# Kernel optimization log

Measured on AMD Instinct MI355X. Metric: run time of the kernel, lower is better.

## Reference

```python
import jax, jax.numpy as jnp
import numpy as np

N = 200000      # total points
B = 4           # number of point clouds
C_IN = 128
C_OUT = 256
GRID = 0.05
EPS = 1e-5      # BatchNorm eps


def setup_inputs() -> dict:
    key = jax.random.key(0)
    ks = jax.random.split(key, 9)
    xyz = jax.random.uniform(ks[0], (1, N, 3), dtype=jnp.float32)
    features = jax.random.normal(ks[1], (1, N, C_IN), dtype=jnp.float32)
    offset = jnp.array([50000, 100000, 150000, 200000], dtype=jnp.int32)
    W1 = jax.random.normal(ks[2], (C_OUT, C_IN), dtype=jnp.float32) * 0.02
    b1 = jax.random.normal(ks[3], (C_OUT,), dtype=jnp.float32) * 0.01
    gamma = jax.random.uniform(ks[4], (C_OUT,), dtype=jnp.float32, minval=0.5, maxval=1.5)
    beta = jax.random.normal(ks[5], (C_OUT,), dtype=jnp.float32) * 0.1
    W2 = jax.random.normal(ks[6], (C_OUT, C_OUT), dtype=jnp.float32) * 0.02
    b2 = jax.random.normal(ks[7], (C_OUT,), dtype=jnp.float32) * 0.01
    return {"xyz": xyz, "features": features, "offset": offset,
            "W1": W1, "b1": b1, "gamma": gamma, "beta": beta, "W2": W2, "b2": b2}


def _offset2batch(offset, n):
    counts = jnp.diff(jnp.concatenate([jnp.zeros((1,), offset.dtype), offset]))
    return jnp.repeat(jnp.arange(offset.shape[0], dtype=jnp.int32), counts,
                      total_repeat_length=n)


def reference(xyz, features, offset, W1, b1, gamma, beta, W2, b2):
    pos = xyz[0]          # [N, 3]
    x = features[0]       # [N, C_IN]
    batch = _offset2batch(offset, pos.shape[0])  # [N]

    # fc: 1x1 conv == linear; BatchNorm1d in training mode (batch stats, biased var)
    h = x @ W1.T + b1                                   # [N, C_OUT]
    mu = h.mean(axis=0)
    var = h.var(axis=0)
    h = (h - mu) / jnp.sqrt(var + EPS) * gamma + beta
    h = jax.nn.relu(h)
    feats = h @ W2.T + b2                               # [N, C_OUT]

    # per-batch min corner (start)
    start = jax.ops.segment_min(pos, batch, num_segments=B)   # [B, 3]

    # voxel grid clustering
    coords = jnp.floor((pos - start[batch]) / GRID).astype(jnp.int32)  # [N, 3] >= 0
    dims = coords.max(axis=0) + 1
    lin = ((batch * dims[0] + coords[:, 0]) * dims[1] + coords[:, 1]) * dims[2] + coords[:, 2]

    uniq, inv, counts = jnp.unique(lin, return_inverse=True, return_counts=True)
    M = uniq.shape[0]

    # segment_csr mean / max over voxels (order-independent, equals sorted CSR reduce)
    xyz_out = jax.ops.segment_sum(pos, inv, num_segments=M) / counts[:, None].astype(pos.dtype)
    feat_out = jax.ops.segment_max(feats, inv, num_segments=M)

    seg_batch = jax.ops.segment_max(batch, inv, num_segments=M)
    offset_out = jnp.cumsum(jnp.bincount(seg_batch, length=B)).astype(offset.dtype)

    return (xyz_out[None], feat_out[None], offset_out, inv)
```

## Files before the change

kernel.cpp:

```cpp
#include <hip/hip_runtime.h>
#include <stdint.h>

#define GRID_SZ 0.05f
#define BN_EPS 1e-5f

typedef __attribute__((ext_vector_type(8))) short bf16x8;
typedef __attribute__((ext_vector_type(4))) float f32x4;

#define WS_START   0
#define WS_DIMS    64
#define WS_CHSUM   128
#define WS_CHSQ    1152
#define WS_AC      2176
#define WS_BC      3200
#define WS_W1B     4224
#define WS_W2B     69760
#define WS_GRAM    200832
#define WS_CSUM    266368
#define WS_HIST    266880
#define WS_RANK    529024
#define WS_CURS    791296
#define WS_BSUM    1053440
#define WS_XYZS    1053952
#define WS_LIN     1840384
#define WS_PERM    2640384
#define WS_XB      3440384

__device__ __forceinline__ short f2bf(float f) {
  unsigned u = __float_as_uint(f);
  u += 0x7FFFu + ((u >> 16) & 1u);
  return (short)(u >> 16);
}

__device__ __forceinline__ bf16x8 load_frag(const float* p) {
  f32x4 a = *(const f32x4*)p;
  f32x4 b = *(const f32x4*)(p + 4);
  bf16x8 r;
  r[0] = f2bf(a[0]); r[1] = f2bf(a[1]); r[2] = f2bf(a[2]); r[3] = f2bf(a[3]);
  r[4] = f2bf(b[0]); r[5] = f2bf(b[1]); r[6] = f2bf(b[2]); r[7] = f2bf(b[3]);
  return r;
}

__device__ __forceinline__ int batch_of(int p, const int* offs, int nb) {
  int b = 0;
  while (b < nb - 1 && p >= offs[b]) b++;
  return b;
}

__global__ void k_conv(const float* __restrict__ src, short* __restrict__ dst, size_t n8) {
  size_t i = (size_t)blockIdx.x * blockDim.x + threadIdx.x;
  size_t stride = (size_t)gridDim.x * blockDim.x;
  for (; i < n8; i += stride)
    *(bf16x8*)(dst + i * 8) = load_frag(src + i * 8);
}

__global__ void k_convw(const float* __restrict__ W1, const float* __restrict__ W2,
                        short* __restrict__ W1b, short* __restrict__ W2b) {
  int i = blockIdx.x * blockDim.x + threadIdx.x;
  if (i < 4096) *(bf16x8*)(W1b + i * 8) = load_frag(W1 + i * 8);
  else { int j = i - 4096; *(bf16x8*)(W2b + j * 8) = load_frag(W2 + j * 8); }
}

__global__ void k_init(unsigned* featU, size_t featN, int* hist, float* xyzs,
                       float* chsum, float* chsq, float* gram, float* csum,
                       unsigned* gstart, int* gdims) {
  size_t i = (size_t)blockIdx.x * blockDim.x + threadIdx.x;
  size_t stride = (size_t)gridDim.x * blockDim.x;
  for (size_t j = i; j < featN; j += stride) featU[j] = 0u;
  for (size_t j = i; j < 65536; j += stride) hist[j] = 0;
  for (size_t j = i; j < 65536u * 3; j += stride) xyzs[j] = 0.f;
  for (size_t j = i; j < 16384; j += stride) gram[j] = 0.f;
  if (i < 256) { chsum[i] = 0.f; chsq[i] = 0.f; }
  if (i < 128) csum[i] = 0.f;
  if (i < 12) gstart[i] = 0x7F800000u;
  if (i < 3) gdims[i] = 0;
}

__global__ void k_min(const float* __restrict__ pos, const int* __restrict__ offs,
                      int N, int nb, unsigned* gstart) {
  __shared__ unsigned smin[12];
  int tid = threadIdx.x;
  if (tid < 12) smin[tid] = 0x7F800000u;
  __syncthreads();
  int p = blockIdx.x * blockDim.x + tid;
  if (p < N) {
    int b = batch_of(p, offs, nb);
    for (int c = 0; c < 3; c++)
      atomicMin(&smin[b * 3 + c], __float_as_uint(pos[p * 3 + c]));
  }
  __syncthreads();
  if (tid < 3 * nb) atomicMin(&gstart[tid], smin[tid]);
}

__global__ void k_dims(const float* __restrict__ pos, const int* __restrict__ offs,
                       int N, int nb, const unsigned* gstart, int* gdims) {
  __shared__ int sd[3];
  int tid = threadIdx.x;
  if (tid < 3) sd[tid] = 0;
  __syncthreads();
  int p = blockIdx.x * blockDim.x + tid;
  if (p < N) {
    int b = batch_of(p, offs, nb);
    for (int c = 0; c < 3; c++) {
      float s = __uint_as_float(gstart[b * 3 + c]);
      int cc = (int)floorf((pos[p * 3 + c] - s) / GRID_SZ);
      atomicMax(&sd[c], cc);
    }
  }
  __syncthreads();
  if (tid < 3) atomicMax(&gdims[tid], sd[tid]);
}

__global__ void k_hist(const float* __restrict__ pos, const int* __restrict__ offs,
                       int N, int nb, const unsigned* gstart, const int* gdims,
                       int* lin, int* hist, float* xyzs) {
  int p = blockIdx.x * blockDim.x + threadIdx.x;
  if (p >= N) return;
  int b = batch_of(p, offs, nb);
  int d0 = gdims[0] + 1, d1 = gdims[1] + 1, d2 = gdims[2] + 1;
  int c[3];
  for (int i = 0; i < 3; i++) {
    float s = __uint_as_float(gstart[b * 3 + i]);
    c[i] = (int)floorf((pos[p * 3 + i] - s) / GRID_SZ);
  }
  int li = ((b * d0 + c[0]) * d1 + c[1]) * d2 + c[2];
  if (li < 0 || li >= 65536) li = 0;
  lin[p] = li;
  atomicAdd(&hist[li], 1);
  atomicAdd(&xyzs[li * 3 + 0], pos[p * 3 + 0]);
  atomicAdd(&xyzs[li * 3 + 1], pos[p * 3 + 1]);
  atomicAdd(&xyzs[li * 3 + 2], pos[p * 3 + 2]);
}

__global__ __launch_bounds__(1024) void k_scanA(const int* __restrict__ hist,
                                                const int* __restrict__ gdims, int nb,
                                                int2* bsum) {
  __shared__ int so[16], sc2[16];
  int d0 = gdims[0] + 1, d1 = gdims[1] + 1, d2 = gdims[2] + 1;
  int bins = nb * d0 * d1 * d2;
  if (bins > 65536) bins = 65536;
  int i = blockIdx.x * 1024 + threadIdx.x;
  int o = 0, c = 0;
  if (i < bins) { int h = hist[i]; o = (h > 0); c = h; }
  for (int d = 1; d < 64; d <<= 1) { o += __shfl_xor(o, d); c += __shfl_xor(c, d); }
  int w = threadIdx.x >> 6;
  if ((threadIdx.x & 63) == 0) { so[w] = o; sc2[w] = c; }
  __syncthreads();
  if (threadIdx.x == 0) {
    int O = 0, C = 0;
    for (int k = 0; k < 16; k++) { O += so[k]; C += sc2[k]; }
    bsum[blockIdx.x] = make_int2(O, C);
  }
}

__global__ __launch_bounds__(1024) void k_scanB(const int* __restrict__ hist,
                                                const int* __restrict__ gdims, int nb,
                                                const int2* __restrict__ bsum,
                                                int* rank, int* cursor) {
  __shared__ int so[1024], sc2[1024];
  __shared__ int sbase[2];
  int d0 = gdims[0] + 1, d1 = gdims[1] + 1, d2 = gdims[2] + 1;
  int bins = nb * d0 * d1 * d2;
  if (bins > 65536) bins = 65536;
  int b = blockIdx.x;
  int tid = threadIdx.x;
  if (tid == 0) {
    int O = 0, C = 0;
    for (int k = 0; k < b; k++) { int2 s = bsum[k]; O += s.x; C += s.y; }
    sbase[0] = O; sbase[1] = C;
  }
  int i = b * 1024 + tid;
  int h = (i < bins) ? hist[i] : 0;
  int o = (h > 0), c = h;
  so[tid] = o; sc2[tid] = c;
  __syncthreads();
  for (int off = 1; off < 1024; off <<= 1) {
    int vo = (tid >= off) ? so[tid - off] : 0;
    int vc = (tid >= off) ? sc2[tid - off] : 0;
    __syncthreads();
    so[tid] += vo; sc2[tid] += vc;
    __syncthreads();
  }
  if (i < bins) {
    rank[i]   = sbase[0] + so[tid] - o;
    cursor[i] = sbase[1] + sc2[tid] - c;
  }
  if (i == bins - 1) rank[bins] = sbase[0] + so[tid];
}

__global__ void k_scatter(const int* __restrict__ lin, const int* __restrict__ rank,
                          int* cursor, int N, int* __restrict__ perm,
                          float* __restrict__ out_inv) {
  int p = blockIdx.x * blockDim.x + threadIdx.x;
  if (p >= N) return;
  int li = lin[p];
  out_inv[p] = (float)rank[li];
  int slot = atomicAdd(&cursor[li], 1);
  perm[slot] = p;
}

__global__ void k_voxfin(const int* __restrict__ hist, const int* __restrict__ rank,
                         const float* __restrict__ xyzs, const int* __restrict__ gdims,
                         int nb, float* out_xyz, float* out_off) {
  int d0 = gdims[0] + 1, d1 = gdims[1] + 1, d2 = gdims[2] + 1;
  int dxyz = d0 * d1 * d2;
  int bins = nb * dxyz;
  if (bins > 65536) bins = 65536;
  int i = blockIdx.x * blockDim.x + threadIdx.x;
  if (blockIdx.x == 0 && (int)threadIdx.x < nb) {
    int t = (int)threadIdx.x;
    int idx = (t + 1) * dxyz; if (idx > bins) idx = bins;
    out_off[t] = (float)rank[idx];
  }
  if (i >= bins) return;
  int cnt = hist[i];
  if (cnt <= 0) return;
  int v = rank[i];
  float fc = (float)cnt;
  out_xyz[v * 3 + 0] = xyzs[i * 3 + 0] / fc;
  out_xyz[v * 3 + 1] = xyzs[i * 3 + 1] / fc;
  out_xyz[v * 3 + 2] = xyzs[i * 3 + 2] / fc;
}

#define GCHUNK 1024
__global__ __launch_bounds__(256, 2) void k_gram(const short* __restrict__ Xb, int N,
                                                 float* __restrict__ gram,
                                                 float* __restrict__ csum) {
  __shared__ short xt[128 * 72];
  __shared__ float lcs[128];
  int tid = threadIdx.x;
  int wid = tid >> 6, lane = tid & 63;
  int lr = lane & 15, lg = lane >> 4;
  int base = blockIdx.x * GCHUNK;
  int cg = tid & 7;
  float cs[16];
#pragma unroll
  for (int j = 0; j < 16; j++) cs[j] = 0.f;
  f32x4 acc[2][8];
#pragma unroll
  for (int a = 0; a < 2; a++)
#pragma unroll
    for (int b = 0; b < 8; b++) acc[a][b] = (f32x4){0.f, 0.f, 0.f, 0.f};

  for (int k0 = 0; k0 < GCHUNK; k0 += 64) {
    __syncthreads();
#pragma unroll
    for (int it = 0; it < 2; it++) {
      int task = tid + it * 256;
      int r = task >> 3;
      int row = base + k0 + r;
      bf16x8 v0 = {0,0,0,0,0,0,0,0}, v1 = {0,0,0,0,0,0,0,0};
      if (row < N) {
        const short* src = Xb + (size_t)row * 128 + cg * 16;
        v0 = *(const bf16x8*)src;
        v1 = *(const bf16x8*)(src + 8);
      }
#pragma unroll
      for (int j = 0; j < 8; j++) {
        cs[j]     += __uint_as_float(((unsigned)(unsigned short)v0[j]) << 16);
        cs[j + 8] += __uint_as_float(((unsigned)(unsigned short)v1[j]) << 16);
      }
      int rs = r ^ (cg << 3);
#pragma unroll
      for (int j = 0; j < 8; j++) {
        xt[(cg * 16 + j) * 72 + rs]     = v0[j];
        xt[(cg * 16 + 8 + j) * 72 + rs] = v1[j];
      }
    }
    __syncthreads();
#pragma unroll
    for (int ks = 0; ks < 2; ks++) {
      int kk = ks * 32 + lg * 8;
      bf16x8 f[8], af[2];
#pragma unroll
      for (int s = 0; s < 8; s++)
        f[s] = *(const bf16x8*)(xt + (s * 16 + lr) * 72 + (kk ^ (s << 3)));
#pragma unroll
      for (int a = 0; a < 2; a++) {
        int ti = wid * 2 + a;
        af[a] = *(const bf16x8*)(xt + (ti * 16 + lr) * 72 + (kk ^ (ti << 3)));
      }
#pragma unroll
      for (int a = 0; a < 2; a++)
#pragma unroll
        for (int b = 0; b < 8; b++)
          acc[a][b] = __builtin_amdgcn_mfma_f32_16x16x32_bf16(af[a], f[b], acc[a][b], 0, 0, 0);
    }
  }
#pragma unroll
  for (int a = 0; a < 2; a++)
#pragma unroll
    for (int b = 0; b < 8; b++)
#pragma unroll
      for (int r_ = 0; r_ < 4; r_++) {
        int ci = (wid * 2 + a) * 16 + lg * 4 + r_;
        int cj = b * 16 + lr;
        atomicAdd(&gram[ci * 128 + cj], acc[a][b][r_]);
      }
  if (tid < 128) lcs[tid] = 0.f;
  __syncthreads();
#pragma unroll
  for (int j = 0; j < 16; j++) atomicAdd(&lcs[cg * 16 + j], cs[j]);
  __syncthreads();
  if (tid < 128) atomicAdd(&csum[tid], lcs[tid]);
}

__global__ __launch_bounds__(128) void k_finalizeG(const float* __restrict__ gram,
                                                   const float* __restrict__ csum,
                                                   const float* __restrict__ W1,
                                                   const float* __restrict__ b1,
                                                   const float* __restrict__ gamma,
                                                   const float* __restrict__ beta,
                                                   int N, float* Ac, float* Bc) {
  __shared__ float w[128], red[128], red2[128];
  int c = blockIdx.x, j = threadIdx.x;
  w[j] = W1[c * 128 + j];
  __syncthreads();
  float t = 0.f;
  for (int k = 0; k < 128; k++) t += gram[k * 128 + j] * w[k];
  red[j]  = t * w[j];
  red2[j] = w[j] * csum[j];
  __syncthreads();
  for (int off = 64; off > 0; off >>= 1) {
    if (j < off) { red[j] += red[j + off]; red2[j] += red2[j + off]; }
    __syncthreads();
  }
  if (j == 0) {
    float fn = (float)N;
    float q  = red[0] / fn;
    float md = red2[0] / fn;
    float b  = b1[c];
    float mu = md + b;
    float e2 = q + 2.f * b * md + b * b;
    float var = e2 - mu * mu;
    float s = gamma[c] * rsqrtf(var + BN_EPS);
    Ac[c] = s;
    Bc[c] = (b - mu) * s + beta[c];
  }
}

template <bool XBF>
__global__ __launch_bounds__(256) void k_statsA(const float* __restrict__ X,
                                                const short* __restrict__ Xb,
                                                const short* __restrict__ W1b,
                                                const float* __restrict__ b1, int N,
                                                float* chsum, float* chsq) {
  int tid = threadIdx.x;
  int wid = tid >> 6, lane = tid & 63;
  int lr = lane & 15, lg = lane >> 4;
  int p0 = blockIdx.x * 64;
  int wcol = wid * 64;
  f32x4 acc[4][4] = {};
  for (int kk = 0; kk < 4; kk++) {
    int k = kk * 32 + lg * 8;
    bf16x8 af[4], bfr[4];
    for (int m = 0; m < 4; m++) {
      int row = p0 + m * 16 + lr; if (row >= N) row = N - 1;
      if (XBF) af[m] = *(const bf16x8*)(Xb + (size_t)row * 128 + k);
      else     af[m] = load_frag(X + (size_t)row * 128 + k);
    }
    for (int n = 0; n < 4; n++)
      bfr[n] = *(const bf16x8*)(W1b + (size_t)(wcol + n * 16 + lr) * 128 + k);
    for (int m = 0; m < 4; m++)
      for (int n = 0; n < 4; n++)
        acc[m][n] = __builtin_amdgcn_mfma_f32_16x16x32_bf16(af[m], bfr[n], acc[m][n], 0, 0, 0);
  }
  for (int n = 0; n < 4; n++) {
    int c = wcol + n * 16 + lr;
    float bv = b1[c];
    float s1 = 0.f, s2 = 0.f;
    for (int m = 0; m < 4; m++)
      for (int r = 0; r < 4; r++) {
        int row = p0 + m * 16 + lg * 4 + r;
        if (row < N) {
          float h = acc[m][n][r] + bv;
          s1 += h; s2 += h * h;
        }
      }
    s1 += __shfl_xor(s1, 16); s2 += __shfl_xor(s2, 16);
    s1 += __shfl_xor(s1, 32); s2 += __shfl_xor(s2, 32);
    if (lg == 0) { atomicAdd(&chsum[c], s1); atomicAdd(&chsq[c], s2); }
  }
}

__global__ void k_finalize(const float* chsum, const float* chsq, const float* b1,
                           const float* gamma, const float* beta, int N,
                           float* Ac, float* Bc) {
  int c = threadIdx.x;
  float fn = (float)N;
  float mu = chsum[c] / fn;
  float var = chsq[c] / fn - mu * mu;
  float s = gamma[c] * rsqrtf(var + BN_EPS);
  Ac[c] = s;
  Bc[c] = (b1[c] - mu) * s + beta[c];
}

template <bool XBF>
__global__ __launch_bounds__(256, 4) void k_gemmB(const float* __restrict__ X,
                                                  const short* __restrict__ Xb,
                                                  const short* __restrict__ W1b,
                                                  const short* __restrict__ W2b,
                                                  const float* __restrict__ b2,
                                                  const float* __restrict__ Ac,
                                                  const float* __restrict__ Bc,
                                                  const int* __restrict__ perm,
                                                  const int* __restrict__ lin,
                                                  const int* __restrict__ rank,
                                                  int N, unsigned* __restrict__ featU) {
  __shared__ char smem[64 * 264 * 2];
  __shared__ int vox_s[64];
  __shared__ int perm_s[64];
  char* ylds = smem;
  unsigned short* lmax = (unsigned short*)smem;

  int tid = threadIdx.x;
  int wid = tid >> 6, lane = tid & 63;
  int lr = lane & 15, lg = lane >> 4;
  int p0 = blockIdx.x * 64;
  int wcol = wid * 64;

  if (tid < 64) {
    int s = p0 + tid;
    int pp = perm[(s < N) ? s : (N - 1)];
    perm_s[tid] = pp;
    vox_s[tid] = (s < N) ? rank[lin[pp]] : -1;
  }
  __syncthreads();

  f32x4 acc[4][4] = {};
  for (int kk = 0; kk < 4; kk++) {
    int k = kk * 32 + lg * 8;
    bf16x8 af[4], bfr[4];
    for (int m = 0; m < 4; m++) {
      int row = perm_s[m * 16 + lr];
      if (XBF) af[m] = *(const bf16x8*)(Xb + (size_t)row * 128 + k);
      else     af[m] = load_frag(X + (size_t)row * 128 + k);
    }
    for (int n = 0; n < 4; n++)
      bfr[n] = *(const bf16x8*)(W1b + (size_t)(wcol + n * 16 + lr) * 128 + k);
    for (int m = 0; m < 4; m++)
      for (int n = 0; n < 4; n++)
        acc[m][n] = __builtin_amdgcn_mfma_f32_16x16x32_bf16(af[m], bfr[n], acc[m][n], 0, 0, 0);
  }

  for (int n = 0; n < 4; n++) {
    int c = wcol + n * 16 + lr;
    float Av = Ac[c], Bv = Bc[c];
    int colb = c * 2;
    for (int m = 0; m < 4; m++)
      for (int r = 0; r < 4; r++) {
        int row = m * 16 + lg * 4 + r;
        float y = fmaxf(acc[m][n][r] * Av + Bv, 0.0f);
        int addr = (row * 512 + colb) ^ ((row & 7) << 4);
        *(short*)(ylds + addr) = f2bf(y);
      }
  }
  __syncthreads();

  f32x4 acc2[4][4] = {};
  for (int kk = 0; kk < 8; kk++) {
    int k = kk * 32 + lg * 8;
    int kb = k * 2;
    bf16x8 af[4], bfr[4];
    for (int m = 0; m < 4; m++) {
      int row = m * 16 + lr;
      af[m] = *(const bf16x8*)(ylds + ((row * 512 + kb) ^ ((row & 7) << 4)));
    }
    for (int n = 0; n < 4; n++)
      bfr[n] = *(const bf16x8*)(W2b + (size_t)(wcol + n * 16 + lr) * 256 + k);
    for (int m = 0; m < 4; m++)
      for (int n = 0; n < 4; n++)
        acc2[m][n] = __builtin_amdgcn_mfma_f32_16x16x32_bf16(af[m], bfr[n], acc2[m][n], 0, 0, 0);
  }
  __syncthreads();

  for (int n = 0; n < 4; n++) {
    int c = wcol + n * 16 + lr;
    float bv = b2[c];
    for (int m = 0; m < 4; m++)
      for (int r = 0; r < 4; r++) {
        int row = m * 16 + lg * 4 + r;
        unsigned us = (unsigned)(unsigned short)f2bf(acc2[m][n][r] + bv);
        us = (us & 0x8000u) ? (~us & 0xFFFFu) : (us | 0x8000u);
        lmax[row * 264 + c] = (unsigned short)us;
      }
  }
  __syncthreads();

  int nrows = N - p0; if (nrows > 64) nrows = 64;
  int c = tid;
  unsigned run = 0;
  int vprev = vox_s[0];
  int run_start = 0;
  for (int row = 0; row < nrows; row++) {
    int v = vox_s[row];
    if (v != vprev) {
      size_t idx = (size_t)vprev * 256 + c;
      if (run_start > 0) featU[idx] = run << 16;
      else atomicMax(&featU[idx], run << 16);
      run = 0; vprev = v; run_start = row;
    }
    run = max(run, (unsigned)lmax[row * 264 + c]);
  }
  atomicMax(&featU[(size_t)vprev * 256 + c], run << 16);
}

__global__ void k_decode(unsigned* featU, size_t n) {
  size_t i = (size_t)blockIdx.x * blockDim.x + threadIdx.x;
  size_t stride = (size_t)gridDim.x * blockDim.x;
  for (; i < n; i += stride) {
    unsigned e = featU[i] >> 16;
    unsigned us = (e & 0x8000u) ? (e & 0x7FFFu) : (~e & 0xFFFFu);
    ((float*)featU)[i] = __uint_as_float(us << 16);
  }
}

extern "C" void kernel_launch(void* const* d_in, const int* in_sizes, int n_in,
                              void* d_out, int out_size, void* d_ws, size_t ws_size,
                              hipStream_t stream) {
  const float* xyz   = (const float*)d_in[0];
  const float* X     = (const float*)d_in[1];
  const int*   offs  = (const int*)d_in[2];
  const float* W1    = (const float*)d_in[3];
  const float* b1    = (const float*)d_in[4];
  const float* gamma = (const float*)d_in[5];
  const float* beta  = (const float*)d_in[6];
  const float* W2    = (const float*)d_in[7];
  const float* b2    = (const float*)d_in[8];

  int N  = in_sizes[0] / 3;
  int nb = in_sizes[2];
  int M  = (out_size - nb - N) / 259;
  if (M <= 0) return;

  char* ws = (char*)d_ws;
  unsigned* gstart = (unsigned*)(ws + WS_START);
  int*   gdims  = (int*)(ws + WS_DIMS);
  float* chsum  = (float*)(ws + WS_CHSUM);
  float* chsq   = (float*)(ws + WS_CHSQ);
  float* Ac     = (float*)(ws + WS_AC);
  float* Bc     = (float*)(ws + WS_BC);
  short* W1b    = (short*)(ws + WS_W1B);
  short* W2b    = (short*)(ws + WS_W2B);
  float* gram   = (float*)(ws + WS_GRAM);
  float* csum   = (float*)(ws + WS_CSUM);
  int*   hist   = (int*)(ws + WS_HIST);
  int*   rank   = (int*)(ws + WS_RANK);
  int*   cursor = (int*)(ws + WS_CURS);
  int2*  bsum   = (int2*)(ws + WS_BSUM);
  float* xyzs   = (float*)(ws + WS_XYZS);
  int*   lin    = (int*)(ws + WS_LIN);
  int*   perm   = (int*)(ws + WS_PERM);
  short* Xb     = (short*)(ws + WS_XB);

  size_t req = (size_t)WS_XB + (size_t)N * 128 * 2;
  bool xbf = ws_size >= req;

  float* out_xyz  = (float*)d_out;
  float* out_feat = out_xyz + (size_t)3 * M;
  float* out_off  = out_feat + (size_t)M * 256;
  float* out_inv  = out_off + nb;
  unsigned* featU = (unsigned*)out_feat;

  int npb = (N + 255) / 256;
  int ngb = (N + 63) / 64;
  int ngr = (N + GCHUNK - 1) / GCHUNK;

  hipLaunchKernelGGL(k_init, dim3(2048), dim3(256), 0, stream,
                     featU, (size_t)M * 256, hist, xyzs, chsum, chsq, gram, csum,
                     gstart, gdims);
  hipLaunchKernelGGL(k_convw, dim3(24), dim3(256), 0, stream, W1, W2, W1b, W2b);
  if (xbf) {
    hipLaunchKernelGGL(k_conv, dim3(4096), dim3(256), 0, stream, X, Xb, (size_t)N * 128 / 8);
    hipLaunchKernelGGL(k_gram, dim3(ngr), dim3(256), 0, stream, Xb, N, gram, csum);
  }
  hipLaunchKernelGGL(k_min, dim3(npb), dim3(256), 0, stream, xyz, offs, N, nb, gstart);
  hipLaunchKernelGGL(k_dims, dim3(npb), dim3(256), 0, stream, xyz, offs, N, nb, gstart, gdims);
  hipLaunchKernelGGL(k_hist, dim3(npb), dim3(256), 0, stream,
                     xyz, offs, N, nb, gstart, gdims, lin, hist, xyzs);
  hipLaunchKernelGGL(k_scanA, dim3(64), dim3(1024), 0, stream, hist, gdims, nb, bsum);
  hipLaunchKernelGGL(k_scanB, dim3(64), dim3(1024), 0, stream,
                     hist, gdims, nb, bsum, rank, cursor);
  hipLaunchKernelGGL(k_voxfin, dim3(256), dim3(256), 0, stream,
                     hist, rank, xyzs, gdims, nb, out_xyz, out_off);
  hipLaunchKernelGGL(k_scatter, dim3(npb), dim3(256), 0, stream,
                     lin, rank, cursor, N, perm, out_inv);
  if (xbf) {
    hipLaunchKernelGGL(k_finalizeG, dim3(256), dim3(128), 0, stream,
                       gram, csum, W1, b1, gamma, beta, N, Ac, Bc);
    hipLaunchKernelGGL((k_gemmB<true>), dim3(ngb), dim3(256), 0, stream,
                       X, Xb, W1b, W2b, b2, Ac, Bc, perm, lin, rank, N, featU);
  } else {
    hipLaunchKernelGGL((k_statsA<false>), dim3(ngb), dim3(256), 0, stream,
                       X, Xb, W1b, b1, N, chsum, chsq);
    hipLaunchKernelGGL(k_finalize, dim3(1), dim3(256), 0, stream,
                       chsum, chsq, b1, gamma, beta, N, Ac, Bc);
    hipLaunchKernelGGL((k_gemmB<false>), dim3(ngb), dim3(256), 0, stream,
                       X, Xb, W1b, W2b, b2, Ac, Bc, perm, lin, rank, N, featU);
  }
  hipLaunchKernelGGL(k_decode, dim3(2048), dim3(256), 0, stream,
                     featU, (size_t)M * 256);
}
```

Before: 323.5 us.

## Fuse X bf16 conversion into gram kernel, fold weight conversion into init

The separate fp32-to-bf16 conversion pass over X is merged into the Gram-matrix kernel, which now reads fp32 X, writes Xb and accumulates the Gram sums in one pass. This removes one full read of the bf16 copy and two kernel launches, since weight conversion is also folded into k_init. k_min and k_dims replace shared-memory atomics with wavefront shuffle reductions and one global atomic per wave. gemmB launch bounds change from 4 to 3 waves per SIMD, which gives more registers per thread but lower occupancy.

```diff
diff --git a/kernel.cpp b/kernel.cpp
--- a/kernel.cpp
+++ b/kernel.cpp
@@ -47,25 +47,15 @@
   return b;
 }
 
-__global__ void k_conv(const float* __restrict__ src, short* __restrict__ dst, size_t n8) {
+__global__ void k_init(unsigned* featU, size_t featN, int* hist, float* xyzs,
+                       float* chsum, float* chsq, float* gram, float* csum,
+                       unsigned* gstart, int* gdims,
+                       const float* __restrict__ W1, const float* __restrict__ W2,
+                       short* __restrict__ W1b, short* __restrict__ W2b) {
   size_t i = (size_t)blockIdx.x * blockDim.x + threadIdx.x;
   size_t stride = (size_t)gridDim.x * blockDim.x;
-  for (; i < n8; i += stride)
-    *(bf16x8*)(dst + i * 8) = load_frag(src + i * 8);
-}
-
-__global__ void k_convw(const float* __restrict__ W1, const float* __restrict__ W2,
-                        short* __restrict__ W1b, short* __restrict__ W2b) {
-  int i = blockIdx.x * blockDim.x + threadIdx.x;
   if (i < 4096) *(bf16x8*)(W1b + i * 8) = load_frag(W1 + i * 8);
-  else { int j = i - 4096; *(bf16x8*)(W2b + j * 8) = load_frag(W2 + j * 8); }
-}
-
-__global__ void k_init(unsigned* featU, size_t featN, int* hist, float* xyzs,
-                       float* chsum, float* chsq, float* gram, float* csum,
-                       unsigned* gstart, int* gdims) {
-  size_t i = (size_t)blockIdx.x * blockDim.x + threadIdx.x;
-  size_t stride = (size_t)gridDim.x * blockDim.x;
+  else if (i < 12288) { size_t j = i - 4096; *(bf16x8*)(W2b + j * 8) = load_frag(W2 + j * 8); }
   for (size_t j = i; j < featN; j += stride) featU[j] = 0u;
   for (size_t j = i; j < 65536; j += stride) hist[j] = 0;
   for (size_t j = i; j < 65536u * 3; j += stride) xyzs[j] = 0.f;
@@ -78,37 +68,55 @@
 
 __global__ void k_min(const float* __restrict__ pos, const int* __restrict__ offs,
                       int N, int nb, unsigned* gstart) {
-  __shared__ unsigned smin[12];
-  int tid = threadIdx.x;
-  if (tid < 12) smin[tid] = 0x7F800000u;
-  __syncthreads();
-  int p = blockIdx.x * blockDim.x + tid;
+  int p = blockIdx.x * blockDim.x + threadIdx.x;
+  int lane = threadIdx.x & 63;
+  int b = -1;
+  float v0 = __uint_as_float(0x7F800000u), v1 = v0, v2 = v0;
+  if (p < N) {
+    b = batch_of(p, offs, nb);
+    v0 = pos[p * 3 + 0]; v1 = pos[p * 3 + 1]; v2 = pos[p * 3 + 2];
+  }
+  int b0 = __shfl(b, 0);
+  bool uni = __all(b == b0);
+  if (uni) {
+    for (int d = 1; d < 64; d <<= 1) {
+      v0 = fminf(v0, __shfl_xor(v0, d));
+      v1 = fminf(v1, __shfl_xor(v1, d));
+      v2 = fminf(v2, __shfl_xor(v2, d));
+    }
+    if (lane == 0 && b0 >= 0) {
+      atomicMin(&gstart[b0 * 3 + 0], __float_as_uint(v0));
+      atomicMin(&gstart[b0 * 3 + 1], __float_as_uint(v1));
+      atomicMin(&gstart[b0 * 3 + 2], __float_as_uint(v2));
+    }
+  } else if (p < N) {
+    atomicMin(&gstart[b * 3 + 0], __float_as_uint(v0));
+    atomicMin(&gstart[b * 3 + 1], __float_as_uint(v1));
+    atomicMin(&gstart[b * 3 + 2], __float_as_uint(v2));
+  }
+}
+
+__global__ void k_dims(const float* __restrict__ pos, const int* __restrict__ offs,
+                       int N, int nb, const unsigned* gstart, int* gdims) {
+  int p = blockIdx.x * blockDim.x + threadIdx.x;
+  int lane = threadIdx.x & 63;
+  int c0 = 0, c1 = 0, c2 = 0;
   if (p < N) {
     int b = batch_of(p, offs, nb);
-    for (int c = 0; c < 3; c++)
-      atomicMin(&smin[b * 3 + c], __float_as_uint(pos[p * 3 + c]));
-  }
-  __syncthreads();
-  if (tid < 3 * nb) atomicMin(&gstart[tid], smin[tid]);
-}
-
-__global__ void k_dims(const float* __restrict__ pos, const int* __restrict__ offs,
-                       int N, int nb, const unsigned* gstart, int* gdims) {
-  __shared__ int sd[3];
-  int tid = threadIdx.x;
-  if (tid < 3) sd[tid] = 0;
-  __syncthreads();
-  int p = blockIdx.x * blockDim.x + tid;
-  if (p < N) {
-    int b = batch_of(p, offs, nb);
-    for (int c = 0; c < 3; c++) {
-      float s = __uint_as_float(gstart[b * 3 + c]);
-      int cc = (int)floorf((pos[p * 3 + c] - s) / GRID_SZ);
-      atomicMax(&sd[c], cc);
-    }
-  }
-  __syncthreads();
-  if (tid < 3) atomicMax(&gdims[tid], sd[tid]);
+    c0 = (int)floorf((pos[p * 3 + 0] - __uint_as_float(gstart[b * 3 + 0])) / GRID_SZ);
+    c1 = (int)floorf((pos[p * 3 + 1] - __uint_as_float(gstart[b * 3 + 1])) / GRID_SZ);
+    c2 = (int)floorf((pos[p * 3 + 2] - __uint_as_float(gstart[b * 3 + 2])) / GRID_SZ);
+  }
+  for (int d = 1; d < 64; d <<= 1) {
+    c0 = max(c0, __shfl_xor(c0, d));
+    c1 = max(c1, __shfl_xor(c1, d));
+    c2 = max(c2, __shfl_xor(c2, d));
+  }
+  if (lane == 0) {
+    atomicMax(&gdims[0], c0);
+    atomicMax(&gdims[1], c1);
+    atomicMax(&gdims[2], c2);
+  }
 }
 
 __global__ void k_hist(const float* __restrict__ pos, const int* __restrict__ offs,
@@ -223,9 +231,10 @@
 }
 
 #define GCHUNK 1024
-__global__ __launch_bounds__(256, 2) void k_gram(const short* __restrict__ Xb, int N,
-                                                 float* __restrict__ gram,
-                                                 float* __restrict__ csum) {
+__global__ __launch_bounds__(256, 2) void k_convgram(const float* __restrict__ X,
+                                                     short* __restrict__ Xb, int N,
+                                                     float* __restrict__ gram,
+                                                     float* __restrict__ csum) {
   __shared__ short xt[128 * 72];
   __shared__ float lcs[128];
   int tid = threadIdx.x;
@@ -251,9 +260,12 @@
       int row = base + k0 + r;
       bf16x8 v0 = {0,0,0,0,0,0,0,0}, v1 = {0,0,0,0,0,0,0,0};
       if (row < N) {
-        const short* src = Xb + (size_t)row * 128 + cg * 16;
-        v0 = *(const bf16x8*)src;
-        v1 = *(const bf16x8*)(src + 8);
+        const float* src = X + (size_t)row * 128 + cg * 16;
+        v0 = load_frag(src);
+        v1 = load_frag(src + 8);
+        short* dst = Xb + (size_t)row * 128 + cg * 16;
+        *(bf16x8*)dst = v0;
+        *(bf16x8*)(dst + 8) = v1;
       }
 #pragma unroll
       for (int j = 0; j < 8; j++) {
@@ -339,9 +351,7 @@
   }
 }
 
-template <bool XBF>
 __global__ __launch_bounds__(256) void k_statsA(const float* __restrict__ X,
-                                                const short* __restrict__ Xb,
                                                 const short* __restrict__ W1b,
                                                 const float* __restrict__ b1, int N,
                                                 float* chsum, float* chsq) {
@@ -356,8 +366,7 @@
     bf16x8 af[4], bfr[4];
     for (int m = 0; m < 4; m++) {
       int row = p0 + m * 16 + lr; if (row >= N) row = N - 1;
-      if (XBF) af[m] = *(const bf16x8*)(Xb + (size_t)row * 128 + k);
-      else     af[m] = load_frag(X + (size_t)row * 128 + k);
+      af[m] = load_frag(X + (size_t)row * 128 + k);
     }
     for (int n = 0; n < 4; n++)
       bfr[n] = *(const bf16x8*)(W1b + (size_t)(wcol + n * 16 + lr) * 128 + k);
@@ -396,7 +405,7 @@
 }
 
 template <bool XBF>
-__global__ __launch_bounds__(256, 4) void k_gemmB(const float* __restrict__ X,
+__global__ __launch_bounds__(256, 3) void k_gemmB(const float* __restrict__ X,
                                                   const short* __restrict__ Xb,
                                                   const short* __restrict__ W1b,
                                                   const short* __restrict__ W2b,
@@ -568,12 +577,9 @@
 
   hipLaunchKernelGGL(k_init, dim3(2048), dim3(256), 0, stream,
                      featU, (size_t)M * 256, hist, xyzs, chsum, chsq, gram, csum,
-                     gstart, gdims);
-  hipLaunchKernelGGL(k_convw, dim3(24), dim3(256), 0, stream, W1, W2, W1b, W2b);
-  if (xbf) {
-    hipLaunchKernelGGL(k_conv, dim3(4096), dim3(256), 0, stream, X, Xb, (size_t)N * 128 / 8);
-    hipLaunchKernelGGL(k_gram, dim3(ngr), dim3(256), 0, stream, Xb, N, gram, csum);
-  }
+                     gstart, gdims, W1, W2, W1b, W2b);
+  if (xbf)
+    hipLaunchKernelGGL(k_convgram, dim3(ngr), dim3(256), 0, stream, X, Xb, N, gram, csum);
   hipLaunchKernelGGL(k_min, dim3(npb), dim3(256), 0, stream, xyz, offs, N, nb, gstart);
   hipLaunchKernelGGL(k_dims, dim3(npb), dim3(256), 0, stream, xyz, offs, N, nb, gstart, gdims);
   hipLaunchKernelGGL(k_hist, dim3(npb), dim3(256), 0, stream,
@@ -591,8 +597,8 @@
     hipLaunchKernelGGL((k_gemmB<true>), dim3(ngb), dim3(256), 0, stream,
                        X, Xb, W1b, W2b, b2, Ac, Bc, perm, lin, rank, N, featU);
   } else {
-    hipLaunchKernelGGL((k_statsA<false>), dim3(ngb), dim3(256), 0, stream,
-                       X, Xb, W1b, b1, N, chsum, chsq);
+    hipLaunchKernelGGL(k_statsA, dim3(ngb), dim3(256), 0, stream,
+                       X, W1b, b1, N, chsum, chsq);
     hipLaunchKernelGGL(k_finalize, dim3(1), dim3(256), 0, stream,
                        chsum, chsq, b1, gamma, beta, N, Ac, Bc);
     hipLaunchKernelGGL((k_gemmB<false>), dim3(ngb), dim3(256), 0, stream,
```

Measured after the change: 488.8 us. 1.51x slower.
